# Kernel tuning notes

Hardware: AMD Instinct MI355X
Metric: run time of the kernel (lower is better)

## Reference

```python
import jax, jax.numpy as jnp
import numpy as np

N_HEADS = 16
N_KV_HEADS = 4
HEAD_DIM = 128
ROPE_THETA = 10000.0


def _rope_cos_sin(seq_len, head_dim, dtype):
    inv_freq = 1.0 / (ROPE_THETA ** (jnp.arange(0, head_dim, 2, dtype=jnp.float32) / head_dim))
    angles = jnp.arange(seq_len, dtype=jnp.float32)[:, None] * inv_freq[None, :]  # [S, hd/2]
    return jnp.cos(angles).astype(dtype), jnp.sin(angles).astype(dtype)


def _apply_rope(t, cos, sin):
    # t: [B, S, H, hd]; interleaved-pair (complex) rotation, Llama style
    B, S, H, hd = t.shape
    tr = t.reshape(B, S, H, hd // 2, 2)
    t0, t1 = tr[..., 0], tr[..., 1]
    c = cos[None, :, None, :]
    s = sin[None, :, None, :]
    out = jnp.stack([t0 * c - t1 * s, t0 * s + t1 * c], axis=-1)
    return out.reshape(B, S, H, hd)


def setup_inputs() -> dict:
    key = jax.random.key(0)
    ks = jax.random.split(key, 5)
    B, S, D = 2, 2048, 2048
    scale = 0.02
    return {
        "x": jax.random.normal(ks[0], (B, S, D), dtype=jnp.float32),
        "wq": jax.random.normal(ks[1], (N_HEADS * HEAD_DIM, D), dtype=jnp.float32) * scale,
        "wk": jax.random.normal(ks[2], (N_KV_HEADS * HEAD_DIM, D), dtype=jnp.float32) * scale,
        "wv": jax.random.normal(ks[3], (N_KV_HEADS * HEAD_DIM, D), dtype=jnp.float32) * scale,
        "wo": jax.random.normal(ks[4], (D, N_HEADS * HEAD_DIM), dtype=jnp.float32) * scale,
    }


def reference(x, wq, wk, wv, wo):
    B, S, D = x.shape
    hd = HEAD_DIM
    # QKV projections (torch Linear: y = x @ W.T)
    q = (x @ wq.T).reshape(B, S, N_HEADS, hd)
    k = (x @ wk.T).reshape(B, S, N_KV_HEADS, hd)
    v = (x @ wv.T).reshape(B, S, N_KV_HEADS, hd)
    # RoPE on q, k
    cos, sin = _rope_cos_sin(S, hd, x.dtype)
    q = _apply_rope(q, cos, sin)
    k = _apply_rope(k, cos, sin)
    # GQA: repeat kv heads to match query heads
    rep = N_HEADS // N_KV_HEADS
    k = jnp.repeat(k, rep, axis=2)  # [B, S, H, hd]
    v = jnp.repeat(v, rep, axis=2)
    # Causal SDPA
    scores = jnp.einsum("bqhd,bkhd->bhqk", q, k) / jnp.sqrt(jnp.asarray(hd, x.dtype))
    causal = jnp.tril(jnp.ones((S, S), dtype=bool))
    scores = jnp.where(causal[None, None], scores, jnp.asarray(-1e30, x.dtype))
    attn = jax.nn.softmax(scores, axis=-1)
    out = jnp.einsum("bhqk,bkhd->bqhd", attn, v).reshape(B, S, N_HEADS * hd)
    return out @ wo.T
```

## Files before the change

kernel.cpp:

```cpp
#include <hip/hip_runtime.h>
#include <stdint.h>

typedef unsigned short u16;
typedef __attribute__((ext_vector_type(8))) __bf16 bf16x8;
typedef __attribute__((ext_vector_type(4))) float f32x4;

__device__ __forceinline__ u16 f2bf(float f) {
  union { float f; uint32_t u; } v; v.f = f;
  uint32_t u = v.u;
  uint32_t r = (u + 0x7fffu + ((u >> 16) & 1u)) >> 16;
  return (u16)r;
}
__device__ __forceinline__ float bf2f(u16 h) {
  union { uint32_t u; float f; } v; v.u = ((uint32_t)h) << 16;
  return v.f;
}

__device__ __forceinline__ void gld16(const void* g, void* l) {
  __builtin_amdgcn_global_load_lds(
      (__attribute__((address_space(1))) void*)(uintptr_t)g,
      (__attribute__((address_space(3))) void*)l,
      16, 0, 0);
}

__global__ __launch_bounds__(256) void cast_all(const float* __restrict__ x,
                                                const float* __restrict__ wq,
                                                const float* __restrict__ wk,
                                                const float* __restrict__ wv,
                                                const float* __restrict__ wo,
                                                u16* __restrict__ xb,
                                                u16* __restrict__ wqkv,
                                                u16* __restrict__ wob) {
  int i = blockIdx.x * 256 + threadIdx.x;
  const float* src; u16* dst; int loc, base;
  if (i < 2097152)      { src = x;  dst = xb;   loc = i;           base = 0; }
  else if (i < 3145728) { src = wq; dst = wqkv; loc = i - 2097152; base = 0; }
  else if (i < 3407872) { src = wk; dst = wqkv; loc = i - 3145728; base = 1048576; }
  else if (i < 3670016) { src = wv; dst = wqkv; loc = i - 3407872; base = 1310720; }
  else                  { src = wo; dst = wob;  loc = i - 3670016; base = 0; }
  float4 f = ((const float4*)src)[loc];
  ushort4 o;
  o.x = f2bf(f.x); o.y = f2bf(f.y); o.z = f2bf(f.z); o.w = f2bf(f.w);
  ((ushort4*)dst)[base + loc] = o;
}

__global__ __launch_bounds__(256) void gemm_bt(const u16* __restrict__ A,
                                               const u16* __restrict__ B,
                                               void* __restrict__ C,
                                               int M, int N, int K, int out_f32)
{
  __shared__ u16 As[128 * 64];
  __shared__ u16 Bs[128 * 64];
  const int tid  = threadIdx.x;
  const int wave = tid >> 6, lane = tid & 63;
  const int col  = lane & 15, quad = lane >> 4;
  const int bm = blockIdx.y, bn = blockIdx.x;
  const int wm = (wave >> 1) * 64, wn = (wave & 1) * 64;
  const size_t arow0 = (size_t)bm * 128, brow0 = (size_t)bn * 128;

  const int sr = lane >> 3, pc = lane & 7;

  const f32x4 fz = {0.f, 0.f, 0.f, 0.f};
  f32x4 acc[4][4];
  for (int i = 0; i < 4; ++i)
    for (int j = 0; j < 4; ++j) acc[i][j] = fz;

  for (int k0 = 0; k0 < K; k0 += 64) {
    __syncthreads();
    #pragma unroll
    for (int i = 0; i < 4; ++i) {
      int rA = wave * 32 + i * 8 + sr;
      int lc = pc ^ (rA & 7);
      gld16(A + (arow0 + rA) * K + k0 + lc * 8, As + (wave * 32 + i * 8) * 64);
      gld16(B + (brow0 + rA) * K + k0 + lc * 8, Bs + (wave * 32 + i * 8) * 64);
    }
    __syncthreads();
    #pragma unroll
    for (int kk = 0; kk < 2; ++kk) {
      const int swz = (((kk * 4 + quad) ^ (col & 7)) * 8);
      bf16x8 af[4];
      #pragma unroll
      for (int mt = 0; mt < 4; ++mt)
        af[mt] = *(const bf16x8*)&As[(wm + mt * 16 + col) * 64 + swz];
      #pragma unroll
      for (int nt = 0; nt < 4; ++nt) {
        bf16x8 bf = *(const bf16x8*)&Bs[(wn + nt * 16 + col) * 64 + swz];
        #pragma unroll
        for (int mt = 0; mt < 4; ++mt)
          acc[mt][nt] = __builtin_amdgcn_mfma_f32_16x16x32_bf16(af[mt], bf, acc[mt][nt], 0, 0, 0);
      }
    }
  }

  #pragma unroll
  for (int mt = 0; mt < 4; ++mt)
    #pragma unroll
    for (int nt = 0; nt < 4; ++nt)
      #pragma unroll
      for (int i = 0; i < 4; ++i) {
        size_t grow = arow0 + wm + mt * 16 + quad * 4 + i;
        size_t gcol = brow0 + wn + nt * 16 + col;
        float v = acc[mt][nt][i];
        if (out_f32) ((float*)C)[grow * N + gcol] = v;
        else         ((u16*)C)[grow * N + gcol]   = f2bf(v);
      }
}

__global__ __launch_bounds__(256) void rope_kernel(u16* __restrict__ t, int S, float qscale) {
  int idx = blockIdx.x * 256 + threadIdx.x;
  int i = idx & 63;
  int r = idx >> 6;
  int hh = r % 20; r /= 20;
  int s = r % S;
  int b = r / S;
  float inv = exp2f(-(float)i * 0.20762050593046f);
  float ang = (float)s * inv;
  float sn, cs;
  __sincosf(ang, &sn, &cs);
  int colb = (hh < 16) ? hh * 128 : 2048 + (hh - 16) * 128;
  float osc = (hh < 16) ? qscale : 1.0f;
  size_t base = (size_t)(b * S + s) * 3072 + colb + 2 * i;
  float t0 = bf2f(t[base]), t1 = bf2f(t[base + 1]);
  t[base]     = f2bf((t0 * cs - t1 * sn) * osc);
  t[base + 1] = f2bf((t0 * sn + t1 * cs) * osc);
}

__global__ __launch_bounds__(256) void vtrans_kernel(const u16* __restrict__ qkv,
                                                     u16* __restrict__ Vtg, int S) {
  __shared__ u16 T[64 * 65];
  const int s0 = blockIdx.x * 64, d0 = blockIdx.y * 64, bk = blockIdx.z;
  const int b = bk >> 2, kvh = bk & 3;
  const u16* src = qkv + (size_t)b * S * 3072 + 2560 + kvh * 128 + d0;
  #pragma unroll 4
  for (int it = 0; it < 16; ++it) {
    int idx = it * 256 + threadIdx.x;
    int r = idx >> 6, c = idx & 63;
    T[c * 65 + r] = src[(size_t)(s0 + r) * 3072 + c];
  }
  __syncthreads();
  #pragma unroll 4
  for (int it = 0; it < 16; ++it) {
    int idx = it * 256 + threadIdx.x;
    int d = idx >> 6, s = idx & 63;
    Vtg[((size_t)bk * 128 + d0 + d) * S + s0 + s] = T[d * 65 + s];
  }
}

__global__ __launch_bounds__(256, 2) void attn_kernel(const u16* __restrict__ QKV,
                                                      const u16* __restrict__ Vtg,
                                                      u16* __restrict__ Ctx,
                                                      int B, int S)
{
  const int x = blockIdx.x;
  const int t = x >> 5, bh = x & 31;
  const int qt = (x < 256) ? (15 - t) : (t - 8);
  const int h = bh & 15, b = bh >> 4;
  const int tid  = threadIdx.x;
  const int wave = tid >> 6, lane = tid & 63;
  const int col  = lane & 15, quad = lane >> 4;
  const int q0   = qt * 128;
  const int kvh  = h >> 2;
  const int row0w = q0 + wave * 32;

  __shared__ u16 Ks[64 * 128];
  __shared__ u16 Vt[128 * 64];
  __shared__ u16 Ps[4][32 * 72];

  bf16x8 aq[2][4];
  #pragma unroll
  for (int mt = 0; mt < 2; ++mt)
    #pragma unroll
    for (int ks = 0; ks < 4; ++ks)
      aq[mt][ks] = *(const bf16x8*)(QKV + (size_t)(b * S + row0w + mt * 16 + col) * 3072
                                        + h * 128 + ks * 32 + quad * 8);

  const u16* KVb = QKV + (size_t)b * S * 3072 + 2048 + kvh * 128;
  const u16* Vtb = Vtg + ((size_t)(b * 4 + kvh) * 128) * S;
  u16* Pw = Ps[wave];

  const f32x4 fz = {0.f, 0.f, 0.f, 0.f};
  f32x4 o[2][8];
  #pragma unroll
  for (int mt = 0; mt < 2; ++mt)
    #pragma unroll
    for (int nc = 0; nc < 8; ++nc) o[mt][nc] = fz;
  float rs[2] = {0.f, 0.f};

  const int kt_max = 2 * qt + 1;

  for (int kt = 0; kt <= kt_max; ++kt) {
    __syncthreads();
    #pragma unroll
    for (int i = 0; i < 4; ++i) {
      int r = wave * 16 + i * 4 + (lane >> 4);
      int lc = (lane & 15) ^ (r & 15);
      gld16(KVb + (size_t)(kt * 64 + r) * 3072 + lc * 8, Ks + (wave * 16 + i * 4) * 128);
    }
    #pragma unroll
    for (int i = 0; i < 4; ++i) {
      int r = wave * 32 + i * 8 + (lane >> 3);
      int lc = (lane & 7) ^ (r & 7);
      gld16(Vtb + (size_t)r * S + kt * 64 + lc * 8, Vt + (wave * 32 + i * 8) * 64);
    }
    __syncthreads();

    if (kt * 64 > row0w + 31) continue;
    const bool need_mask = (kt * 64 + 63 > row0w);

    #pragma unroll
    for (int nt = 0; nt < 4; ++nt) {
      bf16x8 kA[4];
      #pragma unroll
      for (int ks = 0; ks < 4; ++ks)
        kA[ks] = *(const bf16x8*)&Ks[(nt * 16 + col) * 128 + (((ks * 4 + quad) ^ col) * 8)];
      #pragma unroll
      for (int mt = 0; mt < 2; ++mt) {
        f32x4 st = fz;
        #pragma unroll
        for (int ks = 0; ks < 4; ++ks)
          st = __builtin_amdgcn_mfma_f32_16x16x32_bf16(kA[ks], aq[mt][ks], st, 0, 0, 0);
        float pv[4];
        const int kbase = kt * 64 + nt * 16 + quad * 4;
        const int qrow  = row0w + mt * 16 + col;
        #pragma unroll
        for (int i = 0; i < 4; ++i) {
          float s = st[i];
          if (need_mask && (kbase + i > qrow)) s = -__builtin_inff();
          pv[i] = exp2f(s);
        }
        rs[mt] += (pv[0] + pv[1]) + (pv[2] + pv[3]);
        uint32_t d0 = (__float_as_uint(pv[0]) >> 16) | (__float_as_uint(pv[1]) & 0xffff0000u);
        uint32_t d1 = (__float_as_uint(pv[2]) >> 16) | (__float_as_uint(pv[3]) & 0xffff0000u);
        uint2 dd; dd.x = d0; dd.y = d1;
        *(uint2*)&Pw[(mt * 16 + col) * 72 + nt * 16 + quad * 4] = dd;
      }
    }
    __asm__ volatile("" ::: "memory");

    bf16x8 ap[2][2];
    #pragma unroll
    for (int mt = 0; mt < 2; ++mt)
      #pragma unroll
      for (int ks = 0; ks < 2; ++ks)
        ap[mt][ks] = *(const bf16x8*)&Pw[(mt * 16 + col) * 72 + ks * 32 + quad * 8];
    #pragma unroll
    for (int nc = 0; nc < 8; ++nc) {
      #pragma unroll
      for (int ks = 0; ks < 2; ++ks) {
        bf16x8 bv = *(const bf16x8*)&Vt[(nc * 16 + col) * 64 + (((ks * 4 + quad) ^ (col & 7)) * 8)];
        #pragma unroll
        for (int mt = 0; mt < 2; ++mt)
          o[mt][nc] = __builtin_amdgcn_mfma_f32_16x16x32_bf16(ap[mt][ks], bv, o[mt][nc], 0, 0, 0);
      }
    }
  }

  #pragma unroll
  for (int mt = 0; mt < 2; ++mt) {
    float v = rs[mt];
    v += __shfl_xor(v, 16);
    v += __shfl_xor(v, 32);
    float lv[4];
    #pragma unroll
    for (int i = 0; i < 4; ++i)
      lv[i] = 1.0f / __shfl(v, quad * 4 + i);
    #pragma unroll
    for (int nc = 0; nc < 8; ++nc)
      #pragma unroll
      for (int i = 0; i < 4; ++i) {
        int qg = row0w + mt * 16 + quad * 4 + i;
        Ctx[(size_t)(b * S + qg) * 2048 + h * 128 + nc * 16 + col] =
            f2bf(o[mt][nc][i] * lv[i]);
      }
  }
}

extern "C" void kernel_launch(void* const* d_in, const int* in_sizes, int n_in,
                              void* d_out, int out_size, void* d_ws, size_t ws_size,
                              hipStream_t stream) {
  const int B = 2, S = 2048, D = 2048;
  const int M = B * S;
  const int NQKV = 3072;

  const float* x  = (const float*)d_in[0];
  const float* wq = (const float*)d_in[1];
  const float* wk = (const float*)d_in[2];
  const float* wv = (const float*)d_in[3];
  const float* wo = (const float*)d_in[4];

  char* ws = (char*)d_ws;
  u16* xb    = (u16*)ws; ws += (size_t)M * D * 2;
  u16* wqkvb = (u16*)ws; ws += (size_t)NQKV * D * 2;
  u16* wob   = (u16*)ws; ws += (size_t)D * D * 2;
  u16* qkvb  = (u16*)ws; ws += (size_t)M * NQKV * 2;
  u16* vtg   = (u16*)ws; ws += (size_t)B * 4 * 128 * S * 2;
  u16* ctx   = (u16*)ws; ws += (size_t)M * D * 2;

  cast_all<<<18432, 256, 0, stream>>>(x, wq, wk, wv, wo, xb, wqkvb, wob);

  gemm_bt<<<dim3(NQKV / 128, M / 128), 256, 0, stream>>>(xb, wqkvb, qkvb, M, NQKV, D, 0);

  const float qscale = 0.12751744515623627f;
  rope_kernel<<<(M * 20 * 64) / 256, 256, 0, stream>>>(qkvb, S, qscale);

  vtrans_kernel<<<dim3(S / 64, 2, B * 4), 256, 0, stream>>>(qkvb, vtg, S);

  attn_kernel<<<512, 256, 0, stream>>>(qkvb, vtg, ctx, B, S);

  gemm_bt<<<dim3(D / 128, M / 128), 256, 0, stream>>>(ctx, wob, d_out, M, D, D, 1);
}
```

Before: 298.7 us.

## Double-buffer K tiles and overlap V load with QK^T compute in attention

The K tile now lives in a two-slot LDS buffer. The next K tile is prefetched while the current one is consumed, and the V tile load is issued at the start of each iteration and waited on only before the PV matmul, using explicit vmcnt waits and raw barriers. MFMA blocks are bracketed with s_setprio to favour matrix issue. This aims to hide global-to-LDS latency behind the score and softmax work, at the cost of more LDS, which may reduce occupancy. The hand-counted vmcnt values are fragile and would need to match the number of outstanding loads exactly.

```diff
diff --git a/kernel.cpp b/kernel.cpp
--- a/kernel.cpp
+++ b/kernel.cpp
@@ -162,7 +162,7 @@
   const int kvh  = h >> 2;
   const int row0w = q0 + wave * 32;
 
-  __shared__ u16 Ks[64 * 128];
+  __shared__ u16 Ks[2][64 * 128];
   __shared__ u16 Vt[128 * 64];
   __shared__ u16 Ps[4][32 * 72];
 
@@ -173,6 +173,11 @@
     for (int ks = 0; ks < 4; ++ks)
       aq[mt][ks] = *(const bf16x8*)(QKV + (size_t)(b * S + row0w + mt * 16 + col) * 3072
                                         + h * 128 + ks * 32 + quad * 8);
+  #pragma unroll
+  for (int mt = 0; mt < 2; ++mt)
+    #pragma unroll
+    for (int ks = 0; ks < 4; ++ks)
+      asm volatile("" :: "v"(__builtin_bit_cast(f32x4, aq[mt][ks])));
 
   const u16* KVb = QKV + (size_t)b * S * 3072 + 2048 + kvh * 128;
   const u16* Vtb = Vtg + ((size_t)(b * 4 + kvh) * 128) * S;
@@ -188,71 +193,96 @@
 
   const int kt_max = 2 * qt + 1;
 
+  #pragma unroll
+  for (int i = 0; i < 4; ++i) {
+    int r = wave * 16 + i * 4 + (lane >> 4);
+    int lc = (lane & 15) ^ (r & 15);
+    gld16(KVb + (size_t)r * 3072 + lc * 8, Ks[0] + (wave * 16 + i * 4) * 128);
+  }
+
   for (int kt = 0; kt <= kt_max; ++kt) {
-    __syncthreads();
-    #pragma unroll
-    for (int i = 0; i < 4; ++i) {
-      int r = wave * 16 + i * 4 + (lane >> 4);
-      int lc = (lane & 15) ^ (r & 15);
-      gld16(KVb + (size_t)(kt * 64 + r) * 3072 + lc * 8, Ks + (wave * 16 + i * 4) * 128);
-    }
     #pragma unroll
     for (int i = 0; i < 4; ++i) {
       int r = wave * 32 + i * 8 + (lane >> 3);
       int lc = (lane & 7) ^ (r & 7);
       gld16(Vtb + (size_t)r * S + kt * 64 + lc * 8, Vt + (wave * 32 + i * 8) * 64);
     }
-    __syncthreads();
-
-    if (kt * 64 > row0w + 31) continue;
+    {
+      int ktn = (kt < kt_max) ? kt + 1 : kt;
+      u16* kdst = Ks[(kt + 1) & 1];
+      #pragma unroll
+      for (int i = 0; i < 4; ++i) {
+        int r = wave * 16 + i * 4 + (lane >> 4);
+        int lc = (lane & 15) ^ (r & 15);
+        gld16(KVb + (size_t)(ktn * 64 + r) * 3072 + lc * 8, kdst + (wave * 16 + i * 4) * 128);
+      }
+    }
+
+    asm volatile("s_waitcnt vmcnt(8)" ::: "memory");
+    __builtin_amdgcn_s_barrier();
+
+    const u16* Kc = Ks[kt & 1];
+    const bool active = (kt * 64 <= row0w + 31);
     const bool need_mask = (kt * 64 + 63 > row0w);
 
-    #pragma unroll
-    for (int nt = 0; nt < 4; ++nt) {
-      bf16x8 kA[4];
-      #pragma unroll
-      for (int ks = 0; ks < 4; ++ks)
-        kA[ks] = *(const bf16x8*)&Ks[(nt * 16 + col) * 128 + (((ks * 4 + quad) ^ col) * 8)];
-      #pragma unroll
-      for (int mt = 0; mt < 2; ++mt) {
-        f32x4 st = fz;
+    bf16x8 ap[2][2];
+    if (active) {
+      #pragma unroll
+      for (int nt = 0; nt < 4; ++nt) {
+        bf16x8 kA[4];
         #pragma unroll
         for (int ks = 0; ks < 4; ++ks)
-          st = __builtin_amdgcn_mfma_f32_16x16x32_bf16(kA[ks], aq[mt][ks], st, 0, 0, 0);
-        float pv[4];
-        const int kbase = kt * 64 + nt * 16 + quad * 4;
-        const int qrow  = row0w + mt * 16 + col;
-        #pragma unroll
-        for (int i = 0; i < 4; ++i) {
-          float s = st[i];
-          if (need_mask && (kbase + i > qrow)) s = -__builtin_inff();
-          pv[i] = exp2f(s);
+          kA[ks] = *(const bf16x8*)&Kc[(nt * 16 + col) * 128 + (((ks * 4 + quad) ^ col) * 8)];
+        #pragma unroll
+        for (int mt = 0; mt < 2; ++mt) {
+          f32x4 st = fz;
+          __builtin_amdgcn_s_setprio(1);
+          #pragma unroll
+          for (int ks = 0; ks < 4; ++ks)
+            st = __builtin_amdgcn_mfma_f32_16x16x32_bf16(kA[ks], aq[mt][ks], st, 0, 0, 0);
+          __builtin_amdgcn_s_setprio(0);
+          float pv[4];
+          const int kbase = kt * 64 + nt * 16 + quad * 4;
+          const int qrow  = row0w + mt * 16 + col;
+          #pragma unroll
+          for (int i = 0; i < 4; ++i) {
+            float s = st[i];
+            if (need_mask && (kbase + i > qrow)) s = -__builtin_inff();
+            pv[i] = exp2f(s);
+          }
+          rs[mt] += (pv[0] + pv[1]) + (pv[2] + pv[3]);
+          uint32_t d0 = (__float_as_uint(pv[0]) >> 16) | (__float_as_uint(pv[1]) & 0xffff0000u);
+          uint32_t d1 = (__float_as_uint(pv[2]) >> 16) | (__float_as_uint(pv[3]) & 0xffff0000u);
+          uint2 dd; dd.x = d0; dd.y = d1;
+          *(uint2*)&Pw[(mt * 16 + col) * 72 + nt * 16 + quad * 4] = dd;
         }
-        rs[mt] += (pv[0] + pv[1]) + (pv[2] + pv[3]);
-        uint32_t d0 = (__float_as_uint(pv[0]) >> 16) | (__float_as_uint(pv[1]) & 0xffff0000u);
-        uint32_t d1 = (__float_as_uint(pv[2]) >> 16) | (__float_as_uint(pv[3]) & 0xffff0000u);
-        uint2 dd; dd.x = d0; dd.y = d1;
-        *(uint2*)&Pw[(mt * 16 + col) * 72 + nt * 16 + quad * 4] = dd;
-      }
-    }
-    __asm__ volatile("" ::: "memory");
-
-    bf16x8 ap[2][2];
-    #pragma unroll
-    for (int mt = 0; mt < 2; ++mt)
-      #pragma unroll
-      for (int ks = 0; ks < 2; ++ks)
-        ap[mt][ks] = *(const bf16x8*)&Pw[(mt * 16 + col) * 72 + ks * 32 + quad * 8];
-    #pragma unroll
-    for (int nc = 0; nc < 8; ++nc) {
-      #pragma unroll
-      for (int ks = 0; ks < 2; ++ks) {
-        bf16x8 bv = *(const bf16x8*)&Vt[(nc * 16 + col) * 64 + (((ks * 4 + quad) ^ (col & 7)) * 8)];
-        #pragma unroll
-        for (int mt = 0; mt < 2; ++mt)
-          o[mt][nc] = __builtin_amdgcn_mfma_f32_16x16x32_bf16(ap[mt][ks], bv, o[mt][nc], 0, 0, 0);
-      }
-    }
+      }
+      __asm__ volatile("" ::: "memory");
+      #pragma unroll
+      for (int mt = 0; mt < 2; ++mt)
+        #pragma unroll
+        for (int ks = 0; ks < 2; ++ks)
+          ap[mt][ks] = *(const bf16x8*)&Pw[(mt * 16 + col) * 72 + ks * 32 + quad * 8];
+    }
+
+    asm volatile("s_waitcnt vmcnt(4)" ::: "memory");
+    __builtin_amdgcn_s_barrier();
+
+    if (active) {
+      #pragma unroll
+      for (int nc = 0; nc < 8; ++nc) {
+        #pragma unroll
+        for (int ks = 0; ks < 2; ++ks) {
+          bf16x8 bv = *(const bf16x8*)&Vt[(nc * 16 + col) * 64 + (((ks * 4 + quad) ^ (col & 7)) * 8)];
+          __builtin_amdgcn_s_setprio(1);
+          #pragma unroll
+          for (int mt = 0; mt < 2; ++mt)
+            o[mt][nc] = __builtin_amdgcn_mfma_f32_16x16x32_bf16(ap[mt][ks], bv, o[mt][nc], 0, 0, 0);
+          __builtin_amdgcn_s_setprio(0);
+        }
+      }
+    }
+    __builtin_amdgcn_s_barrier();
   }
 
   #pragma unroll
```

New measurement: 317.0 us. 1.06x slower.

## Fuse RoPE into QKV GEMM epilogue and remap workgroups across XCDs

Applied to the files above, without the earlier changes.

Removes the standalone RoPE kernel and applies the rotation and query scaling in the QKV GEMM epilogue. The partner element of each pair comes from a lane shuffle, and the rotation is done on fp32 accumulators before the bf16 store. It also remaps the flat workgroup index in a stride-8 pattern so that neighbouring tiles land on the same XCD, aiming for better L2 reuse. This saves a full read-modify-write pass over the Q/K buffer and one launch, at the cost of extra sincos work in the GEMM epilogue.

```diff
diff --git a/kernel.cpp b/kernel.cpp
--- a/kernel.cpp
+++ b/kernel.cpp
@@ -47,14 +47,20 @@
 __global__ __launch_bounds__(256) void gemm_bt(const u16* __restrict__ A,
                                                const u16* __restrict__ B,
                                                void* __restrict__ C,
-                                               int M, int N, int K, int out_f32)
+                                               int M, int N, int K, int out_f32,
+                                               int do_rope)
 {
   __shared__ u16 As[128 * 64];
   __shared__ u16 Bs[128 * 64];
   const int tid  = threadIdx.x;
   const int wave = tid >> 6, lane = tid & 63;
   const int col  = lane & 15, quad = lane >> 4;
-  const int bm = blockIdx.y, bn = blockIdx.x;
+
+  const int nwg = gridDim.x * gridDim.y;
+  int flat = blockIdx.y * gridDim.x + blockIdx.x;
+  int swz  = (nwg & 7) ? flat : ((flat & 7) * (nwg >> 3) + (flat >> 3));
+  const int bm = swz / gridDim.x, bn = swz % gridDim.x;
+
   const int wm = (wave >> 1) * 64, wn = (wave & 1) * 64;
   const size_t arow0 = (size_t)bm * 128, brow0 = (size_t)bn * 128;
 
@@ -77,14 +83,14 @@
     __syncthreads();
     #pragma unroll
     for (int kk = 0; kk < 2; ++kk) {
-      const int swz = (((kk * 4 + quad) ^ (col & 7)) * 8);
+      const int swzk = (((kk * 4 + quad) ^ (col & 7)) * 8);
       bf16x8 af[4];
       #pragma unroll
       for (int mt = 0; mt < 4; ++mt)
-        af[mt] = *(const bf16x8*)&As[(wm + mt * 16 + col) * 64 + swz];
+        af[mt] = *(const bf16x8*)&As[(wm + mt * 16 + col) * 64 + swzk];
       #pragma unroll
       for (int nt = 0; nt < 4; ++nt) {
-        bf16x8 bf = *(const bf16x8*)&Bs[(wn + nt * 16 + col) * 64 + swz];
+        bf16x8 bf = *(const bf16x8*)&Bs[(wn + nt * 16 + col) * 64 + swzk];
         #pragma unroll
         for (int mt = 0; mt < 4; ++mt)
           acc[mt][nt] = __builtin_amdgcn_mfma_f32_16x16x32_bf16(af[mt], bf, acc[mt][nt], 0, 0, 0);
@@ -92,37 +98,32 @@
     }
   }
 
+  const float qscale = 0.12751744515623627f;
   #pragma unroll
   for (int mt = 0; mt < 4; ++mt)
     #pragma unroll
-    for (int nt = 0; nt < 4; ++nt)
+    for (int nt = 0; nt < 4; ++nt) {
+      const size_t gcol = brow0 + wn + nt * 16 + col;
+      const bool rope_here = do_rope && (gcol < 2560);
+      const int  d    = (int)(gcol & 127);
+      const float osc = (gcol < 2048) ? qscale : 1.0f;
+      const float inv = exp2f(-(float)(d >> 1) * 0.20762050593046f);
+      const bool odd  = (d & 1) != 0;
       #pragma unroll
       for (int i = 0; i < 4; ++i) {
         size_t grow = arow0 + wm + mt * 16 + quad * 4 + i;
-        size_t gcol = brow0 + wn + nt * 16 + col;
         float v = acc[mt][nt][i];
+        if (rope_here) {
+          float p = __shfl_xor(v, 1);
+          float ang = (float)(int)(grow & 2047) * inv;
+          float sn, cs;
+          __sincosf(ang, &sn, &cs);
+          v = odd ? (p * sn + v * cs) * osc : (v * cs - p * sn) * osc;
+        }
         if (out_f32) ((float*)C)[grow * N + gcol] = v;
         else         ((u16*)C)[grow * N + gcol]   = f2bf(v);
       }
-}
-
-__global__ __launch_bounds__(256) void rope_kernel(u16* __restrict__ t, int S, float qscale) {
-  int idx = blockIdx.x * 256 + threadIdx.x;
-  int i = idx & 63;
-  int r = idx >> 6;
-  int hh = r % 20; r /= 20;
-  int s = r % S;
-  int b = r / S;
-  float inv = exp2f(-(float)i * 0.20762050593046f);
-  float ang = (float)s * inv;
-  float sn, cs;
-  __sincosf(ang, &sn, &cs);
-  int colb = (hh < 16) ? hh * 128 : 2048 + (hh - 16) * 128;
-  float osc = (hh < 16) ? qscale : 1.0f;
-  size_t base = (size_t)(b * S + s) * 3072 + colb + 2 * i;
-  float t0 = bf2f(t[base]), t1 = bf2f(t[base + 1]);
-  t[base]     = f2bf((t0 * cs - t1 * sn) * osc);
-  t[base + 1] = f2bf((t0 * sn + t1 * cs) * osc);
+    }
 }
 
 __global__ __launch_bounds__(256) void vtrans_kernel(const u16* __restrict__ qkv,
@@ -298,14 +299,11 @@
 
   cast_all<<<18432, 256, 0, stream>>>(x, wq, wk, wv, wo, xb, wqkvb, wob);
 
-  gemm_bt<<<dim3(NQKV / 128, M / 128), 256, 0, stream>>>(xb, wqkvb, qkvb, M, NQKV, D, 0);
-
-  const float qscale = 0.12751744515623627f;
-  rope_kernel<<<(M * 20 * 64) / 256, 256, 0, stream>>>(qkvb, S, qscale);
+  gemm_bt<<<dim3(NQKV / 128, M / 128), 256, 0, stream>>>(xb, wqkvb, qkvb, M, NQKV, D, 0, 1);
 
   vtrans_kernel<<<dim3(S / 64, 2, B * 4), 256, 0, stream>>>(qkvb, vtg, S);
 
   attn_kernel<<<512, 256, 0, stream>>>(qkvb, vtg, ctx, B, S);
 
-  gemm_bt<<<dim3(D / 128, M / 128), 256, 0, stream>>>(ctx, wob, d_out, M, D, D, 1);
-}
+  gemm_bt<<<dim3(D / 128, M / 128), 256, 0, stream>>>(ctx, wob, d_out, M, D, D, 1, 0);
+}
```

After: 296.9 us. Within noise of the previous version (-0.6%).
